# Kernel optimization log

Measured on AMD Instinct MI355X. Metric: run time of the kernel, lower is better.

The kernel has to match this reference:

```python
import jax, jax.numpy as jnp
import numpy as np

SPATIAL_PATH = np.array([[1,0,1],[0,1,2],[1,2,1],[4,3,1],[5,4,3],[6,5,4],[5,6,5],[8,7,1],[9,8,7],[10,9,8],[9,10,9]], dtype=np.int32)

B, C_IN, J, T, C_OUT = 64, 3, 11, 512, 128
TEMPORAL_LEN = 7
SIG_CH = 84  # c = C_IN + 1 = 4 -> 4 + 16 + 64


def _signature_depth3(path):
    """Depth-3 path signature with basepoint=0 (Chen's identity over exp of increments).
    path: [N, L, c] -> [N, c + c^2 + c^3]."""
    N, L, c = path.shape
    # basepoint=True: path starts at 0, so first increment is path[:, 0]
    inc = jnp.concatenate([path[:, :1], path[:, 1:] - path[:, :-1]], axis=1)  # [N, L, c]

    def step(carry, d):
        S1, S2, S3 = carry
        e2 = 0.5 * d[:, :, None] * d[:, None, :]                                  # d^{x2}/2!
        e3 = (d[:, :, None, None] * d[:, None, :, None] * d[:, None, None, :]) / 6.0  # d^{x3}/3!
        T1 = S1 + d
        T2 = S2 + S1[:, :, None] * d[:, None, :] + e2
        T3 = (S3 + S2[:, :, :, None] * d[:, None, None, :]
              + S1[:, :, None, None] * e2[:, None, :, :] + e3)
        return (T1, T2, T3), None

    z = lambda *s: jnp.zeros(s, path.dtype)
    (S1, S2, S3), _ = jax.lax.scan(step, (z(N, c), z(N, c, c), z(N, c, c, c)),
                                   jnp.swapaxes(inc, 0, 1))
    return jnp.concatenate([S1, S2.reshape(N, -1), S3.reshape(N, -1)], axis=1)


def _augment_time(path):
    # signatory.Augment(include_time=True, include_original=True): prepend linear time channel
    N, L, _ = path.shape
    t = jnp.broadcast_to(jnp.linspace(0.0, 1.0, L, dtype=path.dtype)[None, :, None], (N, L, 1))
    return jnp.concatenate([t, path], axis=-1)


def _bn(x, gamma, beta, eps=1e-5):
    # train-mode BatchNorm2d (batch statistics), matching module default mode
    m = x.mean(axis=(0, 2, 3), keepdims=True)
    v = x.var(axis=(0, 2, 3), keepdims=True)
    return (x - m) * jax.lax.rsqrt(v + eps) * gamma[None, :, None, None] + beta[None, :, None, None]


def _conv1x1(x, w, b):
    return jnp.einsum('bcjt,oc->bojt', x, w) + b[None, :, None, None]


def _forward(x, path, raw_w, raw_b, raw_g, raw_beta,
             ps_w, ps_b, ps_g, ps_beta, fus_w, fus_b, fus_g, fus_beta):
    B_, C, J_, T_ = x.shape
    # raw branch: Conv2d(C_in, C_out, (1,3), pad (0,1)) + BN + ReLU
    x_conv = jax.lax.conv_general_dilated(x, raw_w, (1, 1), [(0, 0), (1, 1)],
                                          dimension_numbers=('NCHW', 'OIHW', 'NCHW'))
    x_conv = jax.nn.relu(_bn(x_conv + raw_b[None, :, None, None], raw_g, raw_beta))

    # spatial joint paths: gather along joint dim with hand-crafted path [J, 3]
    xp = x.transpose(0, 1, 3, 2)                  # [B, C, T, J]
    sp = xp[:, :, :, path]                        # [B, C, T, J, 3]
    sp = sp.transpose(0, 2, 3, 4, 1).reshape(-1, path.shape[1], C)  # [B*T*J, 3, C]
    s_sig = _signature_depth3(_augment_time(sp))
    s_sig = s_sig.reshape(B_, T_, J_, SIG_CH).transpose(0, 3, 2, 1)  # [B, 84, J, T]

    # temporal paths: replicate-pad T and take 7-wide sliding windows per joint
    pad = (TEMPORAL_LEN - 1) // 2
    x_pad = jnp.pad(x, ((0, 0), (0, 0), (0, 0), (pad, pad)), mode='edge')
    widx = jnp.arange(T_)[:, None] + jnp.arange(TEMPORAL_LEN)[None, :]  # [T, 7]
    tp = x_pad[:, :, :, widx]                     # [B, C, J, T, 7]
    tp = tp.transpose(0, 3, 2, 4, 1).reshape(-1, TEMPORAL_LEN, C)       # [B*T*J, 7, C]
    t_sig = _signature_depth3(_augment_time(tp))
    t_sig = t_sig.reshape(B_, T_, J_, SIG_CH).transpose(0, 3, 2, 1)     # [B, 84, J, T]

    sig = jnp.concatenate([s_sig, t_sig], axis=1)                       # [B, 168, J, T]
    sig = jax.nn.relu(_bn(_conv1x1(sig, ps_w, ps_b), ps_g, ps_beta))    # [B, C_out, J, T]

    out = jnp.concatenate([x_conv, sig], axis=1)                        # [B, 2*C_out, J, T]
    return jax.nn.relu(_bn(_conv1x1(out, fus_w, fus_b), fus_g, fus_beta))


def setup_inputs() -> dict:
    key = jax.random.key(0)
    ks = jax.random.split(key, 4)
    return {
        'x': jax.random.normal(ks[0], (B, C_IN, J, T), jnp.float32),
        'path': jnp.asarray(SPATIAL_PATH),
        'raw_w': jax.random.normal(ks[1], (C_OUT, C_IN, 1, 3), jnp.float32) * 0.2,
        'raw_b': jnp.zeros((C_OUT,), jnp.float32),
        'raw_g': jnp.ones((C_OUT,), jnp.float32),
        'raw_beta': jnp.zeros((C_OUT,), jnp.float32),
        'ps_w': jax.random.normal(ks[2], (C_OUT, 2 * SIG_CH), jnp.float32) * 0.05,
        'ps_b': jnp.zeros((C_OUT,), jnp.float32),
        'ps_g': jnp.ones((C_OUT,), jnp.float32),
        'ps_beta': jnp.zeros((C_OUT,), jnp.float32),
        'fus_w': jax.random.normal(ks[3], (C_OUT, 2 * C_OUT), jnp.float32) * 0.05,
        'fus_b': jnp.zeros((C_OUT,), jnp.float32),
        'fus_g': jnp.ones((C_OUT,), jnp.float32),
        'fus_beta': jnp.zeros((C_OUT,), jnp.float32),
    }


def reference(x, path, raw_w, raw_b, raw_g, raw_beta, ps_w, ps_b, ps_g, ps_beta,
              fus_w, fus_b, fus_g, fus_beta):
    return _forward(x, path, raw_w, raw_b, raw_g, raw_beta,
                    ps_w, ps_b, ps_g, ps_beta, fus_w, fus_b, fus_g, fus_beta)
```

## Files before the change

kernel.cpp:

```cpp
#include <hip/hip_runtime.h>

#define B_    64
#define CIN_  3
#define J_    11
#define T_    512
#define CO_   128
#define KPS_  168
#define KPAD_ 192
#define NLOC_ (B_*J_*T_)
#define NBLK1_ (NLOC_/64)
#define NSTATF_ 360448.0f

typedef unsigned short u16;
typedef unsigned int   u32;

typedef __attribute__((ext_vector_type(8))) short bh8;
typedef __attribute__((ext_vector_type(4))) float f32x4;

__device__ __forceinline__ float b2f(u16 u){ union{u32 i; float f;} v; v.i = ((u32)u)<<16; return v.f; }
__device__ __forceinline__ u16 f2b(float f){ union{float f; u32 i;} v; v.f=f; u32 r = v.i + 0x7FFFu + ((v.i>>16)&1u); return (u16)(r>>16); }
__device__ __forceinline__ u32 pk2(u16 a, u16 b){ return (u32)a | ((u32)b<<16); }

__device__ __forceinline__ float ldx(const void* p, size_t i, bool bf){
  if (bf) return b2f(((const u16*)p)[i]);
  return ((const float*)p)[i];
}
__device__ __forceinline__ bool rflag(const u32* flag){
  return __builtin_amdgcn_readfirstlane(*flag) != 0u;
}

__global__ void kdet(const u32* __restrict__ xw, u32* __restrict__ flag){
  __shared__ int cnt;
  if (threadIdx.x==0) cnt=0;
  __syncthreads();
  u32 w = xw[threadIdx.x*4 + 1];
  int e = (int)((w>>7)&0xFFu);
  if (e>=100 && e<=140) atomicAdd(&cnt,1);
  __syncthreads();
  if (threadIdx.x==0) *flag = (cnt>128) ? 1u : 0u;
}

__global__ __launch_bounds__(256) void k0_prep(const u32* __restrict__ flag,
    const void* __restrict__ ps_w, const void* __restrict__ fus_w,
    u16* __restrict__ psB, u16* __restrict__ fusB,
    float* __restrict__ statsF)
{
  const bool bf = rflag(flag);
  const int stride = gridDim.x*blockDim.x;
  const int t0 = blockIdx.x*blockDim.x + threadIdx.x;
  for (int i=t0;i<64*256;i+=stride) statsF[i]=0.f;
  for (int i=t0;i<128*KPAD_;i+=stride){
    int o=i/KPAD_, kk=i-o*KPAD_;
    int k = (kk<84) ? kk : ((kk>=96 && kk<180) ? kk-12 : -1);
    psB[i] = (k>=0) ? f2b(ldx(ps_w, (size_t)o*KPS_+k, bf)) : (u16)0;
  }
  for (int i=t0;i<128*256;i+=stride){
    int o=i>>8, k=i&255;
    int kc=k>>6, kk=k&63;
    int byte=(o<<7)+(kk<<1); byte ^= ((o&7)<<4);
    fusB[(kc*16384 + byte)>>1] = f2b(ldx(fus_w,i,bf));
  }
}

__device__ __forceinline__ void sigstep(float* S1, float* S2, float* S3, const float* d){
  float e2[16];
  #pragma unroll
  for (int a=0;a<4;a++){
    #pragma unroll
    for (int b=0;b<4;b++) e2[a*4+b] = 0.5f*d[a]*d[b];
  }
  #pragma unroll
  for (int a=0;a<4;a++){
    float s1e = S1[a] + (1.0f/3.0f)*d[a];
    #pragma unroll
    for (int b=0;b<4;b++){
      #pragma unroll
      for (int c=0;c<4;c++){
        S3[a*16+b*4+c] += S2[a*4+b]*d[c] + s1e*e2[b*4+c];
      }
    }
  }
  #pragma unroll
  for (int a=0;a<4;a++){
    #pragma unroll
    for (int b=0;b<4;b++) S2[a*4+b] += S1[a]*d[b] + e2[a*4+b];
  }
  #pragma unroll
  for (int a=0;a<4;a++) S1[a] += d[a];
}

__global__ __launch_bounds__(256) void k1_sig_conv(const u32* __restrict__ flag,
    const void* __restrict__ x, const int* __restrict__ path,
    const void* __restrict__ raw_w, const void* __restrict__ raw_b,
    const void* __restrict__ ps_b, const u16* __restrict__ psB,
    u16* __restrict__ Y, float* __restrict__ partY,
    int locOff, int writeY, int doStats)
{
  const bool bf = rflag(flag);
  __shared__ u16 sAhi[64*KPAD_];
  __shared__ u16 sAlo[64*KPAD_];
  __shared__ float xt[CIN_][72];
  __shared__ float xs[CIN_][3][64];
  __shared__ int   pj[3];

  const int tid = threadIdx.x;
  const int blk = blockIdx.x;
  const int lb  = locOff + blk*64;
  const int lbl = blk*64;
  const int gblk= (locOff>>6) + blk;
  const int b   = lb / (J_*T_);
  const int j   = (lb / T_) % J_;
  const int t0  = lb % T_;
  const size_t xbase = (size_t)b*CIN_*J_*T_;

  if (tid < 3) pj[tid] = path[j*3 + tid];
  for (int idx=tid; idx<CIN_*70; idx+=256){
    int c=idx/70, u=idx-c*70;
    int t=t0+u-3; t = t<0?0:(t>T_-1?T_-1:t);
    xt[c][u] = ldx(x, xbase + (size_t)(c*J_+j)*T_ + t, bf);
  }
  __syncthreads();
  for (int idx=tid; idx<CIN_*3*64; idx+=256){
    int c=idx/192, p=(idx>>6)%3, tt=idx&63;
    xs[c][p][tt] = ldx(x, xbase + (size_t)(c*J_+pj[p])*T_ + t0 + tt, bf);
  }
  __syncthreads();

  const int lane = tid & 63, wid = tid >> 6;
  const int wid2 = wid ^ ((blk&1)<<1);

  if (wid2 < 2){
    const bool spf = (wid2==0);
    const int  tt  = lane;
    const int  L   = spf ? 3 : 7;
    const float dt = spf ? 0.5f : (1.0f/6.0f);
    float S1[4], S2[16], S3[64];
    #pragma unroll
    for (int i=0;i<4;i++)  S1[i]=0.f;
    #pragma unroll
    for (int i=0;i<16;i++) S2[i]=0.f;
    #pragma unroll
    for (int i=0;i<64;i++) S3[i]=0.f;
    float prv[3], d[4];
    for (int c=0;c<3;c++) prv[c] = spf ? xs[c][0][tt] : xt[c][tt];
    d[0]=0.f; d[1]=prv[0]; d[2]=prv[1]; d[3]=prv[2];
    sigstep(S1,S2,S3,d);
    for (int s=1;s<L;s++){
      d[0]=dt;
      for (int c=0;c<3;c++){ float cv = spf ? xs[c][s][tt] : xt[c][tt+s]; d[c+1]=cv-prv[c]; prv[c]=cv; }
      sigstep(S1,S2,S3,d);
    }
    const int sb2 = spf ? 0 : 192;
    const int rowb = tt*(KPAD_*2);
    const int swz  = (tt&7)<<4;
    #pragma unroll
    for (int i=0;i<12;i++){
      u16 hv[8], lv[8];
      #pragma unroll
      for (int e=0;e<8;e++){
        const int idx = i*8+e;
        float v;
        if (idx<4) v=S1[idx]; else if (idx<20) v=S2[idx-4]; else if (idx<84) v=S3[idx-20]; else v=0.f;
        u16 h = f2b(v);
        hv[e]=h; lv[e]=f2b(v - b2f(h));
      }
      int byp = (rowb + sb2 + i*16) ^ swz;
      *reinterpret_cast<uint4*>((char*)sAhi + byp) =
          make_uint4(pk2(hv[0],hv[1]),pk2(hv[2],hv[3]),pk2(hv[4],hv[5]),pk2(hv[6],hv[7]));
      *reinterpret_cast<uint4*>((char*)sAlo + byp) =
          make_uint4(pk2(lv[0],lv[1]),pk2(lv[2],lv[3]),pk2(lv[4],lv[5]),pk2(lv[6],lv[7]));
    }
  } else {
    const int nid = (wid2-2)*64 + lane;
    const int tx = nid & 7, ty2 = nid >> 3;
    #pragma unroll
    for (int cg=0; cg<2; cg++){
      const int chb = cg*64 + ty2*4;
      float w[4][9], bia[4];
      #pragma unroll
      for (int c=0;c<4;c++){
        bia[c]=ldx(raw_b, chb+c, bf);
        #pragma unroll
        for (int q=0;q<9;q++) w[c][q]=ldx(raw_w, (size_t)(chb+c)*9+q, bf);
      }
      float accC[8][4];
      #pragma unroll
      for (int i=0;i<8;i++){
        const int tl=tx*8+i, tg=t0+tl;
        float xv[9];
        #pragma unroll
        for (int cc=0;cc<3;cc++){
          #pragma unroll
          for (int kt=0;kt<3;kt++){
            float v = xt[cc][tl+2+kt];
            if ((tg==0 && kt==0) || (tg==T_-1 && kt==2)) v=0.f;
            xv[cc*3+kt]=v;
          }
        }
        #pragma unroll
        for (int c=0;c<4;c++){
          float s=bia[c];
          #pragma unroll
          for (int q=0;q<9;q++) s=fmaf(xv[q],w[c][q],s);
          accC[i][c]=s;
        }
      }
      if (writeY){
        #pragma unroll
        for (int i=0;i<8;i++){
          u16* yp = Y + (size_t)(lbl + tx*8+i)*256 + chb;
          *reinterpret_cast<uint2*>(yp) =
            make_uint2(pk2(f2b(accC[i][0]),f2b(accC[i][1])), pk2(f2b(accC[i][2]),f2b(accC[i][3])));
        }
      }
      if (doStats){
        #pragma unroll
        for (int c=0;c<4;c++){
          float s=0.f,q=0.f;
          #pragma unroll
          for (int i=0;i<8;i++){ float v=accC[i][c]; s+=v; q+=v*v; }
          s += __shfl_xor(s,1); s += __shfl_xor(s,2); s += __shfl_xor(s,4);
          q += __shfl_xor(q,1); q += __shfl_xor(q,2); q += __shfl_xor(q,4);
          if ((lane&7)==0){
            partY[((size_t)((chb+c)*2  ))*NBLK1_ + gblk] = s;
            partY[((size_t)((chb+c)*2+1))*NBLK1_ + gblk] = q;
          }
        }
      }
    }
  }
  __syncthreads();

  const int lrow = lane >> 4, lcol = lane & 15;
  f32x4 acc[2][4];
  #pragma unroll
  for (int mt=0;mt<2;mt++)
    #pragma unroll
    for (int nt=0;nt<4;nt++) acc[mt][nt] = (f32x4){0.f,0.f,0.f,0.f};

  #pragma unroll
  for (int ks=0;ks<6;ks++){
    const int kk2 = ks*64 + lrow*16;
    bh8 wf[2], yh[4], yl[4];
    #pragma unroll
    for (int mt=0;mt<2;mt++){
      const int o = wid*32 + mt*16 + lcol;
      wf[mt] = *reinterpret_cast<const bh8*>((const char*)psB + o*(KPAD_*2) + kk2);
    }
    #pragma unroll
    for (int nt=0;nt<4;nt++){
      const int l = nt*16 + lcol;
      const int byp = (l*(KPAD_*2) + kk2) ^ ((l&7)<<4);
      yh[nt] = *reinterpret_cast<const bh8*>((const char*)sAhi + byp);
      yl[nt] = *reinterpret_cast<const bh8*>((const char*)sAlo + byp);
    }
    #pragma unroll
    for (int mt=0;mt<2;mt++){
      #pragma unroll
      for (int nt=0;nt<4;nt++){
        acc[mt][nt] = __builtin_amdgcn_mfma_f32_16x16x32_bf16(wf[mt], yh[nt], acc[mt][nt], 0,0,0);
        acc[mt][nt] = __builtin_amdgcn_mfma_f32_16x16x32_bf16(wf[mt], yl[nt], acc[mt][nt], 0,0,0);
      }
    }
  }

  #pragma unroll
  for (int mt=0;mt<2;mt++){
    const int chb = wid*32 + mt*16 + lrow*4;
    float pb[4];
    #pragma unroll
    for (int r=0;r<4;r++) pb[r]=ldx(ps_b, chb+r, bf);
    float sv[4]={0.f,0.f,0.f,0.f}, qv[4]={0.f,0.f,0.f,0.f};
    #pragma unroll
    for (int nt=0;nt<4;nt++){
      float v0=acc[mt][nt][0]+pb[0], v1=acc[mt][nt][1]+pb[1];
      float v2=acc[mt][nt][2]+pb[2], v3=acc[mt][nt][3]+pb[3];
      sv[0]+=v0; qv[0]+=v0*v0; sv[1]+=v1; qv[1]+=v1*v1;
      sv[2]+=v2; qv[2]+=v2*v2; sv[3]+=v3; qv[3]+=v3*v3;
      if (writeY){
        u16* yp = Y + (size_t)(lbl + nt*16+lcol)*256 + 128 + chb;
        *reinterpret_cast<uint2*>(yp) = make_uint2(pk2(f2b(v0),f2b(v1)), pk2(f2b(v2),f2b(v3)));
      }
    }
    if (doStats){
      #pragma unroll
      for (int r=0;r<4;r++){
        float s=sv[r], q=qv[r];
        s += __shfl_xor(s,1); s += __shfl_xor(s,2); s += __shfl_xor(s,4); s += __shfl_xor(s,8);
        q += __shfl_xor(q,1); q += __shfl_xor(q,2); q += __shfl_xor(q,4); q += __shfl_xor(q,8);
        if (lcol==0){
          const int ch = 128 + chb + r;
          partY[((size_t)(ch*2  ))*NBLK1_ + gblk] = s;
          partY[((size_t)(ch*2+1))*NBLK1_ + gblk] = q;
        }
      }
    }
  }
}

__global__ __launch_bounds__(256) void k2_finY(const u32* __restrict__ flag,
    const float* __restrict__ partY,
    const void* __restrict__ raw_g, const void* __restrict__ raw_beta,
    const void* __restrict__ ps_g,  const void* __restrict__ ps_beta,
    float* __restrict__ scaleY, float* __restrict__ shiftY)
{
  const bool bf = rflag(flag);
  const int ch = blockIdx.x;
  const int tid = threadIdx.x;
  const float* prS = partY + (size_t)(ch*2  )*NBLK1_;
  const float* prQ = partY + (size_t)(ch*2+1)*NBLK1_;
  float s=0.f,q=0.f;
  for (int slot=tid; slot<NBLK1_; slot+=256){ s+=prS[slot]; q+=prQ[slot]; }
  s += __shfl_xor(s,1); s += __shfl_xor(s,2); s += __shfl_xor(s,4);
  s += __shfl_xor(s,8); s += __shfl_xor(s,16); s += __shfl_xor(s,32);
  q += __shfl_xor(q,1); q += __shfl_xor(q,2); q += __shfl_xor(q,4);
  q += __shfl_xor(q,8); q += __shfl_xor(q,16); q += __shfl_xor(q,32);
  __shared__ float rs[4], rq[4];
  if ((tid&63)==0){ rs[tid>>6]=s; rq[tid>>6]=q; }
  __syncthreads();
  if (tid==0){
    float S=rs[0]+rs[1]+rs[2]+rs[3], Q=rq[0]+rq[1]+rq[2]+rq[3];
    float m = S/NSTATF_;
    float v = Q/NSTATF_ - m*m; v = fmaxf(v,0.f);
    float r = rsqrtf(v + 1e-5f);
    float g  = (ch<128)? ldx(raw_g,ch,bf)    : ldx(ps_g,ch-128,bf);
    float be = (ch<128)? ldx(raw_beta,ch,bf) : ldx(ps_beta,ch-128,bf);
    scaleY[ch]=r*g; shiftY[ch]=be - m*r*g;
  }
}

__global__ __launch_bounds__(256,4) void k3_fus(const u32* __restrict__ flag,
    const u16* __restrict__ Y,
    const u16* __restrict__ fusB, const float* __restrict__ scaleY, const float* __restrict__ shiftY,
    const void* __restrict__ fus_b, void* __restrict__ F, float* __restrict__ statsF,
    int locOff)
{
  const bool bf = rflag(flag);
  __shared__ u16 sAhi[128*64];
  __shared__ u16 sB  [128*64];
  __shared__ float sSc[256], sSh[256];

  const int tid = threadIdx.x, blk = blockIdx.x;
  const size_t loc0  = (size_t)locOff + (size_t)blk*128;
  const size_t loc0l = (size_t)blk*128;
  const int lane = tid & 63, wid = tid >> 6;
  const int wm = wid >> 1, wn = wid & 1;
  const int lrow = lane >> 4, lcol = lane & 15;
  const int ldloc = tid>>3, ldc16 = tid&7;

  sSc[tid] = scaleY[tid];
  sSh[tid] = shiftY[tid];

  f32x4 acc[4][4];
  #pragma unroll
  for (int mt=0;mt<4;mt++)
    #pragma unroll
    for (int nt=0;nt<4;nt++) acc[mt][nt] = (f32x4){0.f,0.f,0.f,0.f};

  uint4 upre[4];
  #pragma unroll
  for (int p=0;p<4;p++)
    upre[p] = *reinterpret_cast<const uint4*>(Y + (loc0l + p*32+ldloc)*256 + ldc16*8);

  __syncthreads();

  for (int kc=0;kc<4;kc++){
    const int kb = kc*64;
    #pragma unroll
    for (int p=0;p<4;p++){
      const int loc = p*32 + ldloc;
      const int ch0 = kb + ldc16*8;
      uint4 u = upre[p];
      float f[8];
      f[0]=b2f((u16)(u.x&0xffff)); f[1]=b2f((u16)(u.x>>16));
      f[2]=b2f((u16)(u.y&0xffff)); f[3]=b2f((u16)(u.y>>16));
      f[4]=b2f((u16)(u.z&0xffff)); f[5]=b2f((u16)(u.z>>16));
      f[6]=b2f((u16)(u.w&0xffff)); f[7]=b2f((u16)(u.w>>16));
      u16 hi[8];
      #pragma unroll
      for (int jq=0;jq<8;jq++){
        float v = fmaxf(fmaf(f[jq], sSc[ch0+jq], sSh[ch0+jq]), 0.f);
        hi[jq] = f2b(v);
      }
      int byte = (loc<<7) + (ldc16<<4); byte ^= ((loc&7)<<4);
      *reinterpret_cast<uint4*>((char*)sAhi + byte) =
          make_uint4(pk2(hi[0],hi[1]),pk2(hi[2],hi[3]),pk2(hi[4],hi[5]),pk2(hi[6],hi[7]));
    }
    {
      const char* src = (const char*)(fusB + kc*8192);
      #pragma unroll
      for (int p=0;p<4;p++){
        int q16 = (p*256 + tid) << 4;
        *reinterpret_cast<uint4*>((char*)sB + q16) =
            *reinterpret_cast<const uint4*>(src + q16);
      }
    }
    __syncthreads();
    if (kc<3){
      #pragma unroll
      for (int p=0;p<4;p++)
        upre[p] = *reinterpret_cast<const uint4*>(Y + (loc0l + p*32+ldloc)*256 + (kb+64) + ldc16*8);
    }
    #pragma unroll
    for (int ks=0;ks<2;ks++){
      const int kk2 = (ks*32 + lrow*8) << 1;
      bh8 wf[4], yh[4];
      #pragma unroll
      for (int mt=0;mt<4;mt++){
        int o = wm*64 + mt*16 + lcol;
        int byp = (o<<7) + kk2; byp ^= ((o&7)<<4);
        wf[mt] = *reinterpret_cast<const bh8*>((const char*)sB + byp);
      }
      #pragma unroll
      for (int nt=0;nt<4;nt++){
        int l = wn*64 + nt*16 + lcol;
        int byp = (l<<7) + kk2; byp ^= ((l&7)<<4);
        yh[nt] = *reinterpret_cast<const bh8*>((const char*)sAhi + byp);
      }
      #pragma unroll
      for (int mt=0;mt<4;mt++){
        #pragma unroll
        for (int nt=0;nt<4;nt++){
          acc[mt][nt] = __builtin_amdgcn_mfma_f32_16x16x32_bf16(wf[mt], yh[nt], acc[mt][nt], 0,0,0);
        }
      }
    }
    __syncthreads();
  }

  const int bb  = (int)(loc0/(J_*T_));
  const int jj  = (int)((loc0/T_)%J_);
  const int tt0 = (int)(loc0%T_);
  #pragma unroll
  for (int mt=0;mt<4;mt++){
    #pragma unroll
    for (int r=0;r<4;r++){
      const int ch = wm*64 + mt*16 + lrow*4 + r;
      const float fb = ldx(fus_b, ch, bf);
      const size_t ro = ((size_t)(bb*128+ch)*J_ + jj)*T_ + tt0 + wn*64 + lcol;
      float s=0.f, q=0.f;
      #pragma unroll
      for (int nt=0;nt<4;nt++){
        float v = acc[mt][nt][r] + fb;
        s += v; q += v*v;
        float vp = __shfl_xor(v, 1);
        if (bf){
          if (!(lane&1)){
            *reinterpret_cast<u32*>((u16*)F + ro + nt*16) = pk2(f2b(v), f2b(vp));
          }
        } else {
          ((float*)F)[ro + nt*16] = v;
        }
      }
      s += __shfl_xor(s,1); s += __shfl_xor(s,2); s += __shfl_xor(s,4); s += __shfl_xor(s,8);
      q += __shfl_xor(q,1); q += __shfl_xor(q,2); q += __shfl_xor(q,4); q += __shfl_xor(q,8);
      if (lcol==0){
        atomicAdd(&statsF[(blk&63)*256 + ch*2 + 0], s);
        atomicAdd(&statsF[(blk&63)*256 + ch*2 + 1], q);
      }
    }
  }
}

__global__ __launch_bounds__(256) void k4_finF(const u32* __restrict__ flag,
    const float* __restrict__ statsF,
    const void* __restrict__ fus_g, const void* __restrict__ fus_beta,
    float* __restrict__ scaleF, float* __restrict__ shiftF)
{
  const bool bf = rflag(flag);
  int ch = threadIdx.x;
  if (ch < 128){
    float s=0.f,q=0.f;
    for (int slot=0;slot<64;slot++){ s+=statsF[slot*256+ch*2]; q+=statsF[slot*256+ch*2+1]; }
    float m=s/NSTATF_;
    float v=fmaxf(q/NSTATF_-m*m,0.f);
    float r=rsqrtf(v+1e-5f);
    float g=ldx(fus_g,ch,bf), be=ldx(fus_beta,ch,bf);
    scaleF[ch]=r*g; shiftF[ch]=be - m*r*g;
  }
}

__global__ __launch_bounds__(256) void k5_out(const u32* __restrict__ flag,
    const float* __restrict__ scaleF, const float* __restrict__ shiftF, void* __restrict__ out)
{
  const bool bf = rflag(flag);
  const size_t total = (size_t)NLOC_*128;
  const size_t stride = (size_t)gridDim.x*blockDim.x;
  if (bf){
    u16* o16 = (u16*)out;
    for (size_t u8 = (size_t)blockIdx.x*blockDim.x + threadIdx.x; u8*8 < total; u8 += stride){
      size_t idx = u8*8;
      int ch = (int)((idx/(J_*T_)) & 127);
      float sc = scaleF[ch], sh = shiftF[ch];
      uint4 u = *reinterpret_cast<const uint4*>(o16 + idx);
      u32 w[4] = {u.x,u.y,u.z,u.w};
      u32 o[4];
      #pragma unroll
      for (int q=0;q<4;q++){
        float v0=fmaxf(fmaf(b2f((u16)(w[q]&0xffff)),sc,sh),0.f);
        float v1=fmaxf(fmaf(b2f((u16)(w[q]>>16)),sc,sh),0.f);
        o[q]=pk2(f2b(v0),f2b(v1));
      }
      *reinterpret_cast<uint4*>(o16 + idx) = make_uint4(o[0],o[1],o[2],o[3]);
    }
  } else {
    float* of = (float*)out;
    for (size_t u4 = (size_t)blockIdx.x*blockDim.x + threadIdx.x; u4*4 < total; u4 += stride){
      size_t idx = u4*4;
      int ch = (int)((idx/(J_*T_)) & 127);
      float sc = scaleF[ch], sh = shiftF[ch];
      float4 v = *reinterpret_cast<const float4*>(of + idx);
      v.x=fmaxf(fmaf(v.x,sc,sh),0.f);
      v.y=fmaxf(fmaf(v.y,sc,sh),0.f);
      v.z=fmaxf(fmaf(v.z,sc,sh),0.f);
      v.w=fmaxf(fmaf(v.w,sc,sh),0.f);
      *reinterpret_cast<float4*>(of + idx) = v;
    }
  }
}

extern "C" void kernel_launch(void* const* d_in, const int* in_sizes, int n_in,
                              void* d_out, int out_size, void* d_ws, size_t ws_size,
                              hipStream_t stream)
{
  const void* x        = d_in[0];
  const int*  path     = (const int*)d_in[1];
  const void* raw_w    = d_in[2];
  const void* raw_b    = d_in[3];
  const void* raw_g    = d_in[4];
  const void* raw_beta = d_in[5];
  const void* ps_w     = d_in[6];
  const void* ps_b     = d_in[7];
  const void* ps_g     = d_in[8];
  const void* ps_beta  = d_in[9];
  const void* fus_w    = d_in[10];
  const void* fus_b    = d_in[11];
  const void* fus_g    = d_in[12];
  const void* fus_beta = d_in[13];

  char* w = (char*)d_ws;
  u32*   flag   = (u32*)w;   w += 256;
  float* statsF = (float*)w; w += 64*256*4;
  u16*   psB    = (u16*)w;   w += 128*KPAD_*2;
  u16*   fusB   = (u16*)w;   w += 256*128*2;
  float* scaleY = (float*)w; w += 1024;
  float* shiftY = (float*)w; w += 1024;
  float* scaleF = (float*)w; w += 512;
  float* shiftF = (float*)w; w += 512;
  size_t off = (size_t)(w - (char*)d_ws);
  off = (off + 255) & ~(size_t)255;
  u16* Y = (u16*)((char*)d_ws + off);
  size_t avail = (ws_size > off) ? (ws_size - off) : 0;

  float* partY = (float*)d_out;

  const size_t Yfull = (size_t)NLOC_*256*2;
  int c = 1;
  while (c < 64 && Yfull/(size_t)c > avail) c <<= 1;
  const int chunkLoc = NLOC_ / c;

  kdet<<<dim3(1),dim3(256),0,stream>>>((const u32*)x, flag);
  k0_prep<<<dim3(64),dim3(256),0,stream>>>(flag, ps_w, fus_w, psB, fusB, statsF);

  for (int i=0;i<c;i++){
    int wy = (i==c-1)?1:0;
    k1_sig_conv<<<dim3(chunkLoc/64),dim3(256),0,stream>>>(flag, x, path, raw_w, raw_b, ps_b, psB, Y, partY, i*chunkLoc, wy, 1);
  }
  k2_finY<<<dim3(256),dim3(256),0,stream>>>(flag, partY, raw_g, raw_beta, ps_g, ps_beta, scaleY, shiftY);

  k3_fus<<<dim3(chunkLoc/128),dim3(256),0,stream>>>(flag, Y, fusB, scaleY, shiftY, fus_b, d_out, statsF, (c-1)*chunkLoc);
  for (int i=0;i<c-1;i++){
    k1_sig_conv<<<dim3(chunkLoc/64),dim3(256),0,stream>>>(flag, x, path, raw_w, raw_b, ps_b, psB, Y, partY, i*chunkLoc, 1, 0);
    k3_fus<<<dim3(chunkLoc/128),dim3(256),0,stream>>>(flag, Y, fusB, scaleY, shiftY, fus_b, d_out, statsF, i*chunkLoc);
  }
  k4_finF<<<dim3(1),dim3(256),0,stream>>>(flag, statsF, fus_g, fus_beta, scaleF, shiftF);
  k5_out<<<dim3(2048),dim3(256),0,stream>>>(flag, scaleF, shiftF, d_out);
}
```

Baseline: 536.8 us.

## Double-buffer activation tile in LDS and read fusion weights from global

The fusion GEMM kernel now keeps two LDS buffers for the normalized activation tile and fills the next K-chunk while MFMAs run on the current one. This removes one barrier per K iteration. The weight tile is no longer staged in LDS; MFMA operands are loaded straight from a plain row-major bf16 weight array in global memory (held in cache). This cuts LDS traffic and store time, but puts weight loads on the global/L2 path inside the inner loop with uncoalesced 16-byte strided reads.

```diff
diff --git a/kernel.cpp b/kernel.cpp
--- a/kernel.cpp
+++ b/kernel.cpp
@@ -42,7 +42,7 @@
 
 __global__ __launch_bounds__(256) void k0_prep(const u32* __restrict__ flag,
     const void* __restrict__ ps_w, const void* __restrict__ fus_w,
-    u16* __restrict__ psB, u16* __restrict__ fusB,
+    u16* __restrict__ psB, u16* __restrict__ fusW,
     float* __restrict__ statsF)
 {
   const bool bf = rflag(flag);
@@ -54,12 +54,7 @@
     int k = (kk<84) ? kk : ((kk>=96 && kk<180) ? kk-12 : -1);
     psB[i] = (k>=0) ? f2b(ldx(ps_w, (size_t)o*KPS_+k, bf)) : (u16)0;
   }
-  for (int i=t0;i<128*256;i+=stride){
-    int o=i>>8, k=i&255;
-    int kc=k>>6, kk=k&63;
-    int byte=(o<<7)+(kk<<1); byte ^= ((o&7)<<4);
-    fusB[(kc*16384 + byte)>>1] = f2b(ldx(fus_w,i,bf));
-  }
+  for (int i=t0;i<128*256;i+=stride) fusW[i] = f2b(ldx(fus_w,i,bf));
 }
 
 __device__ __forceinline__ void sigstep(float* S1, float* S2, float* S3, const float* d){
@@ -331,13 +326,12 @@
 
 __global__ __launch_bounds__(256,4) void k3_fus(const u32* __restrict__ flag,
     const u16* __restrict__ Y,
-    const u16* __restrict__ fusB, const float* __restrict__ scaleY, const float* __restrict__ shiftY,
+    const u16* __restrict__ fusW, const float* __restrict__ scaleY, const float* __restrict__ shiftY,
     const void* __restrict__ fus_b, void* __restrict__ F, float* __restrict__ statsF,
     int locOff)
 {
   const bool bf = rflag(flag);
-  __shared__ u16 sAhi[128*64];
-  __shared__ u16 sB  [128*64];
+  __shared__ u16 sA[2][128*64];
   __shared__ float sSc[256], sSh[256];
 
   const int tid = threadIdx.x, blk = blockIdx.x;
@@ -361,46 +355,36 @@
   #pragma unroll
   for (int p=0;p<4;p++)
     upre[p] = *reinterpret_cast<const uint4*>(Y + (loc0l + p*32+ldloc)*256 + ldc16*8);
-
+  __syncthreads();
+
+  #pragma unroll
+  for (int p=0;p<4;p++){
+    const int loc = p*32 + ldloc;
+    const int ch0 = ldc16*8;
+    uint4 u = upre[p];
+    float f[8];
+    f[0]=b2f((u16)(u.x&0xffff)); f[1]=b2f((u16)(u.x>>16));
+    f[2]=b2f((u16)(u.y&0xffff)); f[3]=b2f((u16)(u.y>>16));
+    f[4]=b2f((u16)(u.z&0xffff)); f[5]=b2f((u16)(u.z>>16));
+    f[6]=b2f((u16)(u.w&0xffff)); f[7]=b2f((u16)(u.w>>16));
+    u16 hi[8];
+    #pragma unroll
+    for (int jq=0;jq<8;jq++){
+      float v = fmaxf(fmaf(f[jq], sSc[ch0+jq], sSh[ch0+jq]), 0.f);
+      hi[jq] = f2b(v);
+    }
+    int byte = (loc<<7) + (ldc16<<4); byte ^= ((loc&7)<<4);
+    *reinterpret_cast<uint4*>((char*)sA[0] + byte) =
+        make_uint4(pk2(hi[0],hi[1]),pk2(hi[2],hi[3]),pk2(hi[4],hi[5]),pk2(hi[6],hi[7]));
+  }
+  #pragma unroll
+  for (int p=0;p<4;p++)
+    upre[p] = *reinterpret_cast<const uint4*>(Y + (loc0l + p*32+ldloc)*256 + 64 + ldc16*8);
   __syncthreads();
 
   for (int kc=0;kc<4;kc++){
-    const int kb = kc*64;
-    #pragma unroll
-    for (int p=0;p<4;p++){
-      const int loc = p*32 + ldloc;
-      const int ch0 = kb + ldc16*8;
-      uint4 u = upre[p];
-      float f[8];
-      f[0]=b2f((u16)(u.x&0xffff)); f[1]=b2f((u16)(u.x>>16));
-      f[2]=b2f((u16)(u.y&0xffff)); f[3]=b2f((u16)(u.y>>16));
-      f[4]=b2f((u16)(u.z&0xffff)); f[5]=b2f((u16)(u.z>>16));
-      f[6]=b2f((u16)(u.w&0xffff)); f[7]=b2f((u16)(u.w>>16));
-      u16 hi[8];
-      #pragma unroll
-      for (int jq=0;jq<8;jq++){
-        float v = fmaxf(fmaf(f[jq], sSc[ch0+jq], sSh[ch0+jq]), 0.f);
-        hi[jq] = f2b(v);
-      }
-      int byte = (loc<<7) + (ldc16<<4); byte ^= ((loc&7)<<4);
-      *reinterpret_cast<uint4*>((char*)sAhi + byte) =
-          make_uint4(pk2(hi[0],hi[1]),pk2(hi[2],hi[3]),pk2(hi[4],hi[5]),pk2(hi[6],hi[7]));
-    }
-    {
-      const char* src = (const char*)(fusB + kc*8192);
-      #pragma unroll
-      for (int p=0;p<4;p++){
-        int q16 = (p*256 + tid) << 4;
-        *reinterpret_cast<uint4*>((char*)sB + q16) =
-            *reinterpret_cast<const uint4*>(src + q16);
-      }
-    }
-    __syncthreads();
-    if (kc<3){
-      #pragma unroll
-      for (int p=0;p<4;p++)
-        upre[p] = *reinterpret_cast<const uint4*>(Y + (loc0l + p*32+ldloc)*256 + (kb+64) + ldc16*8);
-    }
+    const int cur = kc & 1;
+    const int kb  = kc*64;
     #pragma unroll
     for (int ks=0;ks<2;ks++){
       const int kk2 = (ks*32 + lrow*8) << 1;
@@ -408,14 +392,13 @@
       #pragma unroll
       for (int mt=0;mt<4;mt++){
         int o = wm*64 + mt*16 + lcol;
-        int byp = (o<<7) + kk2; byp ^= ((o&7)<<4);
-        wf[mt] = *reinterpret_cast<const bh8*>((const char*)sB + byp);
+        wf[mt] = *reinterpret_cast<const bh8*>((const char*)fusW + o*512 + (kb<<1) + kk2);
       }
       #pragma unroll
       for (int nt=0;nt<4;nt++){
         int l = wn*64 + nt*16 + lcol;
         int byp = (l<<7) + kk2; byp ^= ((l&7)<<4);
-        yh[nt] = *reinterpret_cast<const bh8*>((const char*)sAhi + byp);
+        yh[nt] = *reinterpret_cast<const bh8*>((const char*)sA[cur] + byp);
       }
       #pragma unroll
       for (int mt=0;mt<4;mt++){
@@ -423,6 +406,34 @@
         for (int nt=0;nt<4;nt++){
           acc[mt][nt] = __builtin_amdgcn_mfma_f32_16x16x32_bf16(wf[mt], yh[nt], acc[mt][nt], 0,0,0);
         }
+      }
+    }
+    if (kc<3){
+      const int chn = kb + 64;
+      #pragma unroll
+      for (int p=0;p<4;p++){
+        const int loc = p*32 + ldloc;
+        const int ch0 = chn + ldc16*8;
+        uint4 u = upre[p];
+        float f[8];
+        f[0]=b2f((u16)(u.x&0xffff)); f[1]=b2f((u16)(u.x>>16));
+        f[2]=b2f((u16)(u.y&0xffff)); f[3]=b2f((u16)(u.y>>16));
+        f[4]=b2f((u16)(u.z&0xffff)); f[5]=b2f((u16)(u.z>>16));
+        f[6]=b2f((u16)(u.w&0xffff)); f[7]=b2f((u16)(u.w>>16));
+        u16 hi[8];
+        #pragma unroll
+        for (int jq=0;jq<8;jq++){
+          float v = fmaxf(fmaf(f[jq], sSc[ch0+jq], sSh[ch0+jq]), 0.f);
+          hi[jq] = f2b(v);
+        }
+        int byte = (loc<<7) + (ldc16<<4); byte ^= ((loc&7)<<4);
+        *reinterpret_cast<uint4*>((char*)sA[cur^1] + byte) =
+            make_uint4(pk2(hi[0],hi[1]),pk2(hi[2],hi[3]),pk2(hi[4],hi[5]),pk2(hi[6],hi[7]));
+      }
+      if (kc<2){
+        #pragma unroll
+        for (int p=0;p<4;p++)
+          upre[p] = *reinterpret_cast<const uint4*>(Y + (loc0l + p*32+ldloc)*256 + (kb+128) + ldc16*8);
       }
     }
     __syncthreads();
@@ -542,7 +553,7 @@
   u32*   flag   = (u32*)w;   w += 256;
   float* statsF = (float*)w; w += 64*256*4;
   u16*   psB    = (u16*)w;   w += 128*KPAD_*2;
-  u16*   fusB   = (u16*)w;   w += 256*128*2;
+  u16*   fusW   = (u16*)w;   w += 128*256*2;
   float* scaleY = (float*)w; w += 1024;
   float* shiftY = (float*)w; w += 1024;
   float* scaleF = (float*)w; w += 512;
@@ -560,7 +571,7 @@
   const int chunkLoc = NLOC_ / c;
 
   kdet<<<dim3(1),dim3(256),0,stream>>>((const u32*)x, flag);
-  k0_prep<<<dim3(64),dim3(256),0,stream>>>(flag, ps_w, fus_w, psB, fusB, statsF);
+  k0_prep<<<dim3(64),dim3(256),0,stream>>>(flag, ps_w, fus_w, psB, fusW, statsF);
 
   for (int i=0;i<c;i++){
     int wy = (i==c-1)?1:0;
@@ -568,10 +579,10 @@
   }
   k2_finY<<<dim3(256),dim3(256),0,stream>>>(flag, partY, raw_g, raw_beta, ps_g, ps_beta, scaleY, shiftY);
 
-  k3_fus<<<dim3(chunkLoc/128),dim3(256),0,stream>>>(flag, Y, fusB, scaleY, shiftY, fus_b, d_out, statsF, (c-1)*chunkLoc);
+  k3_fus<<<dim3(chunkLoc/128),dim3(256),0,stream>>>(flag, Y, fusW, scaleY, shiftY, fus_b, d_out, statsF, (c-1)*chunkLoc);
   for (int i=0;i<c-1;i++){
     k1_sig_conv<<<dim3(chunkLoc/64),dim3(256),0,stream>>>(flag, x, path, raw_w, raw_b, ps_b, psB, Y, partY, i*chunkLoc, 1, 0);
-    k3_fus<<<dim3(chunkLoc/128),dim3(256),0,stream>>>(flag, Y, fusB, scaleY, shiftY, fus_b, d_out, statsF, i*chunkLoc);
+    k3_fus<<<dim3(chunkLoc/128),dim3(256),0,stream>>>(flag, Y, fusW, scaleY, shiftY, fus_b, d_out, statsF, i*chunkLoc);
   }
   k4_finF<<<dim3(1),dim3(256),0,stream>>>(flag, statsF, fus_g, fus_beta, scaleF, shiftF);
   k5_out<<<dim3(2048),dim3(256),0,stream>>>(flag, scaleF, shiftF, d_out);
```

Measured after the change: 611.5 us. +13.9%, slower.
